# Kernel tuning notes

Measured on AMD Instinct MI355X. Metric: run time of the kernel, lower is better.

The kernel has to match this reference:

```python
import jax, jax.numpy as jnp
import numpy as np

H = 1024      # hidden_size
NH = 16       # num_attention_heads
KV = 4        # num_key_value_heads
HD = 64       # head_dim
E = 16        # num_experts
K = 2         # num_experts_per_tok
F = 1024      # moe_intermediate_size
EPS = 1e-6
THETA = 10000.0
B, S = 2, 1024


def rmsnorm(x, w):
    v = x.astype(jnp.float32)
    v = v * jax.lax.rsqrt(jnp.mean(v * v, axis=-1, keepdims=True) + EPS)
    return (v * w).astype(x.dtype)


def rotate_half(x):
    h = x.shape[-1] // 2
    return jnp.concatenate([-x[..., h:], x[..., :h]], axis=-1)


def setup_inputs() -> dict:
    key = jax.random.key(0)
    ks = jax.random.split(key, 12)
    s = 0.02
    return {
        "hidden_states": jax.random.normal(ks[0], (B, S, H), jnp.float32),
        "position_ids": jnp.broadcast_to(jnp.arange(S, dtype=jnp.int32), (B, S)),
        "ln1_w": jnp.ones((H,), jnp.float32),
        "ln2_w": jnp.ones((H,), jnp.float32),
        "q_w": jax.random.normal(ks[1], (NH * HD, H), jnp.float32) * s,
        "k_w": jax.random.normal(ks[2], (KV * HD, H), jnp.float32) * s,
        "v_w": jax.random.normal(ks[3], (KV * HD, H), jnp.float32) * s,
        "o_w": jax.random.normal(ks[4], (H, NH * HD), jnp.float32) * s,
        "qn_w": jnp.ones((HD,), jnp.float32),
        "kn_w": jnp.ones((HD,), jnp.float32),
        "gate_w": jax.random.normal(ks[5], (E, H), jnp.float32) * s,
        "w_gate": jax.random.normal(ks[6], (E, F, H), jnp.float32) * s,
        "w_up": jax.random.normal(ks[7], (E, F, H), jnp.float32) * s,
        "w_down": jax.random.normal(ks[8], (E, H, F), jnp.float32) * s,
    }


def reference(hidden_states, position_ids, ln1_w, ln2_w, q_w, k_w, v_w, o_w,
              qn_w, kn_w, gate_w, w_gate, w_up, w_down):
    b, s, _ = hidden_states.shape
    # ---- attention (pre-norm, bidirectional, GQA, RoPE, q/k RMSNorm) ----
    h = rmsnorm(hidden_states, ln1_w)
    q = (h @ q_w.T).reshape(b, s, NH, HD)
    k = (h @ k_w.T).reshape(b, s, KV, HD)
    v = (h @ v_w.T).reshape(b, s, KV, HD)
    q = jnp.swapaxes(rmsnorm(q, qn_w), 1, 2)   # [b,NH,s,HD]
    k = jnp.swapaxes(rmsnorm(k, kn_w), 1, 2)   # [b,KV,s,HD]
    v = jnp.swapaxes(v, 1, 2)
    inv_freq = 1.0 / (THETA ** (jnp.arange(0, HD, 2, dtype=jnp.float32) / HD))
    freqs = position_ids.astype(jnp.float32)[..., None] * inv_freq  # [b,s,HD/2]
    emb = jnp.concatenate([freqs, freqs], axis=-1)                  # [b,s,HD]
    cos = jnp.cos(emb)[:, None]                                     # [b,1,s,HD]
    sin = jnp.sin(emb)[:, None]
    q = q * cos + rotate_half(q) * sin
    k = k * cos + rotate_half(k) * sin
    rep = NH // KV
    k = jnp.repeat(k, rep, axis=1)
    v = jnp.repeat(v, rep, axis=1)
    scores = jnp.einsum('bhqd,bhkd->bhqk', q, k) * (HD ** -0.5)
    attn = jax.nn.softmax(scores.astype(jnp.float32), axis=-1).astype(q.dtype)
    o = jnp.einsum('bhqk,bhkd->bhqd', attn, v)
    o = jnp.swapaxes(o, 1, 2).reshape(b, s, NH * HD) @ o_w.T
    x1 = hidden_states + o
    # ---- sparse MoE (pre-norm, top-k routing, silu-gated experts) ----
    h2 = rmsnorm(x1, ln2_w)
    xf = h2.reshape(-1, H)                                  # [T,H]
    logits = xf @ gate_w.T                                  # [T,E]
    probs = jax.nn.softmax(logits.astype(jnp.float32), axis=-1)
    w, sel = jax.lax.top_k(probs, K)                        # [T,K]
    w = w / jnp.sum(w, axis=-1, keepdims=True)              # norm_topk_prob
    T = xf.shape[0]
    # combine weights scattered into dense [T,E] (zero for unselected experts)
    cw = jnp.zeros((T, E), jnp.float32).at[jnp.arange(T)[:, None], sel].add(w)
    g = jnp.einsum('th,efh->tef', xf, w_gate)
    u = jnp.einsum('th,efh->tef', xf, w_up)
    a = jax.nn.silu(g) * u
    y = jnp.einsum('tef,ehf,te->th', a, w_down, cw.astype(xf.dtype))
    out = x1 + y.reshape(b, s, H)
    return out, logits.reshape(b, s, E)
```

## Files before the change

### kernel.cpp

```cpp
#include <hip/hip_runtime.h>
#include <hip/hip_bf16.h>
#include <math.h>

typedef __bf16 bf16x8 __attribute__((ext_vector_type(8)));
typedef float f32x4 __attribute__((ext_vector_type(4)));

constexpr int HID = 1024;
constexpr int NHEAD = 16;
constexpr int NKV = 4;
constexpr int HDIM = 64;
constexpr int NEXP = 16;
constexpr int FFD = 1024;
constexpr int NB = 2;
constexpr int SEQ = 1024;
constexpr int TOK = NB * SEQ;
constexpr int QKV_N = NHEAD * HDIM + 2 * NKV * HDIM;
constexpr float RMS_EPS = 1e-6f;
constexpr int LDP = 40;
constexpr int PL = 64 * LDP;

__device__ __forceinline__ void split2(float x, __bf16& h1, __bf16& h2) {
  h1 = (__bf16)x;
  h2 = (__bf16)(x - (float)h1);
}

__device__ __forceinline__ void mfma_step3(const __bf16* sm, int wr, int wc,
                                           int lm, int lq, f32x4 (&acc)[2][2]) {
  int ao0 = (wr + lm) * LDP + lq * 8, ao1 = (wr + 16 + lm) * LDP + lq * 8;
  int bo0 = (wc + lm) * LDP + lq * 8, bo1 = (wc + 16 + lm) * LDP + lq * 8;
  bf16x8 a10 = *(const bf16x8*)(sm + ao0),          a11 = *(const bf16x8*)(sm + ao1);
  bf16x8 a20 = *(const bf16x8*)(sm + PL + ao0),     a21 = *(const bf16x8*)(sm + PL + ao1);
  bf16x8 b10 = *(const bf16x8*)(sm + 2 * PL + bo0), b11 = *(const bf16x8*)(sm + 2 * PL + bo1);
  bf16x8 b20 = *(const bf16x8*)(sm + 3 * PL + bo0), b21 = *(const bf16x8*)(sm + 3 * PL + bo1);
#define MF(A, B, i, j) acc[i][j] = __builtin_amdgcn_mfma_f32_16x16x32_bf16(A, B, acc[i][j], 0, 0, 0)
  MF(a10, b10, 0, 0); MF(a10, b11, 0, 1); MF(a11, b10, 1, 0); MF(a11, b11, 1, 1);
  MF(a10, b20, 0, 0); MF(a10, b21, 0, 1); MF(a11, b20, 1, 0); MF(a11, b21, 1, 1);
  MF(a20, b10, 0, 0); MF(a20, b11, 0, 1); MF(a21, b10, 1, 0); MF(a21, b11, 1, 1);
#undef MF
}

__device__ __forceinline__ void cvt8(__bf16* dst, float4 f0, float4 f1) {
  __bf16 tmp[8] __attribute__((aligned(16))) = {
      (__bf16)f0.x, (__bf16)f0.y, (__bf16)f0.z, (__bf16)f0.w,
      (__bf16)f1.x, (__bf16)f1.y, (__bf16)f1.z, (__bf16)f1.w};
  *(int4*)dst = *(const int4*)tmp;
}


__global__ __launch_bounds__(256) void split2_kernel(
    const float* __restrict__ src, __bf16* __restrict__ p1,
    __bf16* __restrict__ p2, int n) {
  int i = (blockIdx.x * 256 + threadIdx.x) * 4;
  if (i >= n) return;
  float4 v = *(const float4*)(src + i);
  __bf16 t1[4] __attribute__((aligned(8))), t2[4] __attribute__((aligned(8)));
  split2(v.x, t1[0], t2[0]);
  split2(v.y, t1[1], t2[1]);
  split2(v.z, t1[2], t2[2]);
  split2(v.w, t1[3], t2[3]);
  *(int2*)(p1 + i) = *(const int2*)t1;
  *(int2*)(p2 + i) = *(const int2*)t2;
}

__global__ __launch_bounds__(256) void rmsnorm_split2_kernel(
    const float* __restrict__ x, const float* __restrict__ w,
    __bf16* __restrict__ p1, __bf16* __restrict__ p2) {
  int row = blockIdx.x;
  const float* xr = x + (size_t)row * HID;
  float4 v = ((const float4*)xr)[threadIdx.x];
  float ss = v.x * v.x + v.y * v.y + v.z * v.z + v.w * v.w;
  for (int off = 32; off; off >>= 1) ss += __shfl_xor(ss, off);
  __shared__ float red[4];
  int lane = threadIdx.x & 63, wid = threadIdx.x >> 6;
  if (lane == 0) red[wid] = ss;
  __syncthreads();
  float tot = red[0] + red[1] + red[2] + red[3];
  float scale = rsqrtf(tot / (float)HID + RMS_EPS);
  float4 wv = ((const float4*)w)[threadIdx.x];
  float o[4] = {v.x * scale * wv.x, v.y * scale * wv.y,
                v.z * scale * wv.z, v.w * scale * wv.w};
  __bf16 t1[4] __attribute__((aligned(8))), t2[4] __attribute__((aligned(8)));
#pragma unroll
  for (int i = 0; i < 4; i++) split2(o[i], t1[i], t2[i]);
  size_t idx = (size_t)row * HID + threadIdx.x * 4;
  *(int2*)(p1 + idx) = *(const int2*)t1;
  *(int2*)(p2 + idx) = *(const int2*)t2;
}

__global__ __launch_bounds__(256) void rmsnorm_dual_kernel(
    const float* __restrict__ x, const float* __restrict__ w,
    float* __restrict__ outf, __bf16* __restrict__ outb) {
  int row = blockIdx.x;
  const float* xr = x + (size_t)row * HID;
  float4 v = ((const float4*)xr)[threadIdx.x];
  float ss = v.x * v.x + v.y * v.y + v.z * v.z + v.w * v.w;
  for (int off = 32; off; off >>= 1) ss += __shfl_xor(ss, off);
  __shared__ float red[4];
  int lane = threadIdx.x & 63, wid = threadIdx.x >> 6;
  if (lane == 0) red[wid] = ss;
  __syncthreads();
  float tot = red[0] + red[1] + red[2] + red[3];
  float scale = rsqrtf(tot / (float)HID + RMS_EPS);
  float4 wv = ((const float4*)w)[threadIdx.x];
  float o[4] = {v.x * scale * wv.x, v.y * scale * wv.y,
                v.z * scale * wv.z, v.w * scale * wv.w};
  size_t idx = (size_t)row * HID + threadIdx.x * 4;
  *(float4*)(outf + idx) = *(const float4*)o;
  __bf16 tb[4] __attribute__((aligned(8)));
#pragma unroll
  for (int i = 0; i < 4; i++) tb[i] = (__bf16)o[i];
  *(int2*)(outb + idx) = *(const int2*)tb;
}

__global__ __launch_bounds__(256) void rope_split_kernel(
    const float* __restrict__ qkv, const int* __restrict__ pos_ids,
    const float* __restrict__ qn_w, const float* __restrict__ kn_w,
    __bf16* __restrict__ qp1, __bf16* __restrict__ qp2,
    __bf16* __restrict__ kp1, __bf16* __restrict__ kp2,
    __bf16* __restrict__ vp1, __bf16* __restrict__ vp2) {
  int t = blockIdx.x;
  int b = t >> 10, s = t & 1023;
  int lane = threadIdx.x & 63, w = threadIdx.x >> 6;
  float pos = (float)pos_ids[t];
  int fi = lane & 31;
  float inv = powf(10000.0f, -((float)(2 * fi)) / 64.0f);
  float cs = cosf(pos * inv), sn = sinf(pos * inv);
  for (int i = 0; i < 6; i++) {
    int hh = w + 4 * i;
    float val = qkv[(size_t)t * QKV_N + hh * 64 + lane];
    __bf16 h1, h2;
    if (hh < 20) {
      float ss = val * val;
      for (int off = 32; off; off >>= 1) ss += __shfl_xor(ss, off);
      float scale = rsqrtf(ss / 64.0f + RMS_EPS);
      float wgt = (hh < 16) ? qn_w[lane] : kn_w[lane];
      val = val * scale * wgt;
      float partner = __shfl_xor(val, 32);
      float rot = (lane < 32) ? -partner : partner;
      val = val * cs + rot * sn;
      split2(val, h1, h2);
      if (hh < 16) {
        size_t idx = (((size_t)b * NHEAD + hh) * SEQ + s) * HDIM + lane;
        qp1[idx] = h1; qp2[idx] = h2;
      } else {
        size_t idx = (((size_t)b * NKV + (hh - 16)) * SEQ + s) * HDIM + lane;
        kp1[idx] = h1; kp2[idx] = h2;
      }
    } else {
      split2(val, h1, h2);
      size_t idx = (((size_t)b * NKV + (hh - 20)) * HDIM + lane) * SEQ + s;
      vp1[idx] = h1; vp2[idx] = h2;
    }
  }
}

__global__ __launch_bounds__(256) void softmax2_kernel(
    const float* __restrict__ sf,
    __bf16* __restrict__ p1, __bf16* __restrict__ p2) {
  size_t roff = (size_t)blockIdx.x * SEQ;
  int tid = threadIdx.x;
  float4 v4 = *(const float4*)(sf + roff + tid * 4);
  float v[4] = {v4.x, v4.y, v4.z, v4.w};
  float mx = fmaxf(fmaxf(v[0], v[1]), fmaxf(v[2], v[3]));
  for (int off = 32; off; off >>= 1) mx = fmaxf(mx, __shfl_xor(mx, off));
  __shared__ float red[4], red2[4];
  int lane = tid & 63, wid = tid >> 6;
  if (lane == 0) red[wid] = mx;
  __syncthreads();
  mx = fmaxf(fmaxf(red[0], red[1]), fmaxf(red[2], red[3]));
  float e[4], sum = 0.f;
#pragma unroll
  for (int i = 0; i < 4; i++) { e[i] = expf(v[i] - mx); sum += e[i]; }
  for (int off = 32; off; off >>= 1) sum += __shfl_xor(sum, off);
  if (lane == 0) red2[wid] = sum;
  __syncthreads();
  sum = red2[0] + red2[1] + red2[2] + red2[3];
  float invs = 1.0f / sum;
  __bf16 t1[4] __attribute__((aligned(8))), t2[4] __attribute__((aligned(8)));
#pragma unroll
  for (int i = 0; i < 4; i++) split2(e[i] * invs, t1[i], t2[i]);
  *(int2*)(p1 + roff + tid * 4) = *(const int2*)t1;
  *(int2*)(p2 + roff + tid * 4) = *(const int2*)t2;
}


__global__ __launch_bounds__(256) void gemm_qkv4(
    const __bf16* __restrict__ a1, const __bf16* __restrict__ a2,
    const __bf16* __restrict__ b1, const __bf16* __restrict__ b2,
    float* __restrict__ qkv) {
  int m0 = blockIdx.x * 64, n0 = blockIdx.y * 64;
  __shared__ __bf16 sm[4 * PL];
  int tid = threadIdx.x, r = tid >> 2, c8 = (tid & 3) * 8;
  size_t aoff = (size_t)(m0 + r) * HID + c8, boff = (size_t)(n0 + r) * HID + c8;
  f32x4 acc[2][2] = {};
  int lane = tid & 63, wid = tid >> 6;
  int wr = (wid >> 1) * 32, wc = (wid & 1) * 32, lq = lane >> 4, lm = lane & 15;
  int sidx = r * LDP + c8;
  int4 ra1, ra2, rb1, rb2;
  auto preload = [&](int k0) {
    ra1 = *(const int4*)(a1 + aoff + k0);
    ra2 = *(const int4*)(a2 + aoff + k0);
    rb1 = *(const int4*)(b1 + boff + k0);
    rb2 = *(const int4*)(b2 + boff + k0);
  };
  auto stage = [&]() {
    *(int4*)&sm[0 * PL + sidx] = ra1;
    *(int4*)&sm[1 * PL + sidx] = ra2;
    *(int4*)&sm[2 * PL + sidx] = rb1;
    *(int4*)&sm[3 * PL + sidx] = rb2;
  };
  preload(0); stage();
  for (int k0 = 0; k0 < HID; k0 += 32) {
    __syncthreads();
    if (k0 + 32 < HID) preload(k0 + 32);
    mfma_step3(sm, wr, wc, lm, lq, acc);
    __syncthreads();
    if (k0 + 32 < HID) stage();
  }
#pragma unroll
  for (int mt = 0; mt < 2; mt++)
#pragma unroll
    for (int nt = 0; nt < 2; nt++)
#pragma unroll
      for (int i = 0; i < 4; i++) {
        int gm = m0 + wr + mt * 16 + lq * 4 + i;
        int gc = n0 + wc + nt * 16 + lm;
        qkv[(size_t)gm * QKV_N + gc] = acc[mt][nt][i];
      }
}

__global__ __launch_bounds__(256) void gemm_scores4(
    const __bf16* __restrict__ qp1, const __bf16* __restrict__ qp2,
    const __bf16* __restrict__ kp1, const __bf16* __restrict__ kp2,
    float* __restrict__ sf, int b, int h0) {
  int hz = blockIdx.z, h = h0 + hz;
  int m0 = blockIdx.x * 64, n0 = blockIdx.y * 64;
  size_t qbase = ((size_t)(b * NHEAD + h)) * SEQ * HDIM;
  size_t kbase = ((size_t)(b * NKV + (h >> 2))) * SEQ * HDIM;
  __shared__ __bf16 sm[4 * PL];
  int tid = threadIdx.x, r = tid >> 2, c8 = (tid & 3) * 8;
  size_t aoff = qbase + (size_t)(m0 + r) * HDIM + c8;
  size_t boff = kbase + (size_t)(n0 + r) * HDIM + c8;
  f32x4 acc[2][2] = {};
  int lane = tid & 63, wid = tid >> 6;
  int wr = (wid >> 1) * 32, wc = (wid & 1) * 32, lq = lane >> 4, lm = lane & 15;
  int sidx = r * LDP + c8;
  int4 ra1, ra2, rb1, rb2;
  auto preload = [&](int k0) {
    ra1 = *(const int4*)(qp1 + aoff + k0);
    ra2 = *(const int4*)(qp2 + aoff + k0);
    rb1 = *(const int4*)(kp1 + boff + k0);
    rb2 = *(const int4*)(kp2 + boff + k0);
  };
  auto stage = [&]() {
    *(int4*)&sm[0 * PL + sidx] = ra1;
    *(int4*)&sm[1 * PL + sidx] = ra2;
    *(int4*)&sm[2 * PL + sidx] = rb1;
    *(int4*)&sm[3 * PL + sidx] = rb2;
  };
  preload(0); stage();
  for (int k0 = 0; k0 < HDIM; k0 += 32) {
    __syncthreads();
    if (k0 + 32 < HDIM) preload(k0 + 32);
    mfma_step3(sm, wr, wc, lm, lq, acc);
    __syncthreads();
    if (k0 + 32 < HDIM) stage();
  }
#pragma unroll
  for (int mt = 0; mt < 2; mt++)
#pragma unroll
    for (int nt = 0; nt < 2; nt++)
#pragma unroll
      for (int i = 0; i < 4; i++) {
        int gm = m0 + wr + mt * 16 + lq * 4 + i;
        int gc = n0 + wc + nt * 16 + lm;
        size_t idx = ((size_t)hz * SEQ + gm) * SEQ + gc;
        sf[idx] = acc[mt][nt][i] * 0.125f;
      }
}

__global__ __launch_bounds__(256) void gemm_pv4(
    const __bf16* __restrict__ s1, const __bf16* __restrict__ s2,
    const __bf16* __restrict__ vp1, const __bf16* __restrict__ vp2,
    __bf16* __restrict__ o1, __bf16* __restrict__ o2,
    int b, int h0) {
  int hz = blockIdx.z, h = h0 + hz;
  int m0 = blockIdx.x * 64;
  size_t pbase = (size_t)hz * SEQ * SEQ;
  size_t vbase = ((size_t)(b * NKV + (h >> 2))) * HDIM * SEQ;
  __shared__ __bf16 sm[4 * PL];
  int tid = threadIdx.x, r = tid >> 2, c8 = (tid & 3) * 8;
  size_t aoff = pbase + (size_t)(m0 + r) * SEQ + c8;
  size_t boff = vbase + (size_t)r * SEQ + c8;
  f32x4 acc[2][2] = {};
  int lane = tid & 63, wid = tid >> 6;
  int wr = (wid >> 1) * 32, wc = (wid & 1) * 32, lq = lane >> 4, lm = lane & 15;
  int sidx = r * LDP + c8;
  int4 ra1, ra2, rb1, rb2;
  auto preload = [&](int k0) {
    ra1 = *(const int4*)(s1 + aoff + k0);
    ra2 = *(const int4*)(s2 + aoff + k0);
    rb1 = *(const int4*)(vp1 + boff + k0);
    rb2 = *(const int4*)(vp2 + boff + k0);
  };
  auto stage = [&]() {
    *(int4*)&sm[0 * PL + sidx] = ra1;
    *(int4*)&sm[1 * PL + sidx] = ra2;
    *(int4*)&sm[2 * PL + sidx] = rb1;
    *(int4*)&sm[3 * PL + sidx] = rb2;
  };
  preload(0); stage();
  for (int k0 = 0; k0 < SEQ; k0 += 32) {
    __syncthreads();
    if (k0 + 32 < SEQ) preload(k0 + 32);
    mfma_step3(sm, wr, wc, lm, lq, acc);
    __syncthreads();
    if (k0 + 32 < SEQ) stage();
  }
#pragma unroll
  for (int mt = 0; mt < 2; mt++)
#pragma unroll
    for (int nt = 0; nt < 2; nt++)
#pragma unroll
      for (int i = 0; i < 4; i++) {
        int gm = m0 + wr + mt * 16 + lq * 4 + i;
        int gc = wc + nt * 16 + lm;
        size_t idx = ((size_t)(b * SEQ + gm)) * HID + h * 64 + gc;
        __bf16 h1_, h2_;
        split2(acc[mt][nt][i], h1_, h2_);
        o1[idx] = h1_; o2[idx] = h2_;
      }
}

__global__ __launch_bounds__(256) void gemm_oproj4(
    const __bf16* __restrict__ a1, const __bf16* __restrict__ a2,
    const __bf16* __restrict__ b1, const __bf16* __restrict__ b2,
    const float* __restrict__ hidden, float* __restrict__ x1, float* __restrict__ outp) {
  int m0 = blockIdx.x * 64, n0 = blockIdx.y * 64;
  __shared__ __bf16 sm[4 * PL];
  int tid = threadIdx.x, r = tid >> 2, c8 = (tid & 3) * 8;
  size_t aoff = (size_t)(m0 + r) * HID + c8, boff = (size_t)(n0 + r) * HID + c8;
  f32x4 acc[2][2] = {};
  int lane = tid & 63, wid = tid >> 6;
  int wr = (wid >> 1) * 32, wc = (wid & 1) * 32, lq = lane >> 4, lm = lane & 15;
  int sidx = r * LDP + c8;
  int4 ra1, ra2, rb1, rb2;
  auto preload = [&](int k0) {
    ra1 = *(const int4*)(a1 + aoff + k0);
    ra2 = *(const int4*)(a2 + aoff + k0);
    rb1 = *(const int4*)(b1 + boff + k0);
    rb2 = *(const int4*)(b2 + boff + k0);
  };
  auto stage = [&]() {
    *(int4*)&sm[0 * PL + sidx] = ra1;
    *(int4*)&sm[1 * PL + sidx] = ra2;
    *(int4*)&sm[2 * PL + sidx] = rb1;
    *(int4*)&sm[3 * PL + sidx] = rb2;
  };
  preload(0); stage();
  for (int k0 = 0; k0 < HID; k0 += 32) {
    __syncthreads();
    if (k0 + 32 < HID) preload(k0 + 32);
    mfma_step3(sm, wr, wc, lm, lq, acc);
    __syncthreads();
    if (k0 + 32 < HID) stage();
  }
#pragma unroll
  for (int mt = 0; mt < 2; mt++)
#pragma unroll
    for (int nt = 0; nt < 2; nt++)
#pragma unroll
      for (int i = 0; i < 4; i++) {
        int gm = m0 + wr + mt * 16 + lq * 4 + i;
        int gc = n0 + wc + nt * 16 + lm;
        size_t idx = (size_t)gm * HID + gc;
        float val = hidden[idx] + acc[mt][nt][i];
        x1[idx] = val;
        outp[idx] = val;
      }
}


__global__ void zero_cnt_kernel(int* cnt) {
  if (threadIdx.x < NEXP) cnt[threadIdx.x] = 0;
}

__global__ __launch_bounds__(64) void gating_kernel(
    const float* __restrict__ h2f, const float* __restrict__ gw,
    float* __restrict__ logits_out, int* __restrict__ cnt,
    int* __restrict__ list, float* __restrict__ wt) {
  int t = blockIdx.x;
  int lane = threadIdx.x;
  const float* xr = h2f + (size_t)t * HID;
  float part[NEXP] = {};
  for (int k = lane; k < HID; k += 64) {
    float xv = xr[k];
#pragma unroll
    for (int e = 0; e < NEXP; e++) part[e] += xv * gw[e * HID + k];
  }
#pragma unroll
  for (int e = 0; e < NEXP; e++)
    for (int off = 32; off; off >>= 1) part[e] += __shfl_xor(part[e], off);
  if (lane < NEXP) logits_out[(size_t)t * NEXP + lane] = part[lane];
  float mx = part[0];
#pragma unroll
  for (int e = 1; e < NEXP; e++) mx = fmaxf(mx, part[e]);
  float pe[NEXP];
#pragma unroll
  for (int e = 0; e < NEXP; e++) pe[e] = expf(part[e] - mx);
  int e0 = 0; float p0 = pe[0];
#pragma unroll
  for (int e = 1; e < NEXP; e++) if (pe[e] > p0) { p0 = pe[e]; e0 = e; }
  int e1 = -1; float p1 = -1.f;
#pragma unroll
  for (int e = 0; e < NEXP; e++) if (e != e0 && pe[e] > p1) { p1 = pe[e]; e1 = e; }
  float wsum = p0 + p1;
  if (lane == 0) {
    int pos0 = atomicAdd(&cnt[e0], 1);
    list[e0 * TOK + pos0] = t;
    wt[e0 * TOK + pos0] = p0 / wsum;
    int pos1 = atomicAdd(&cnt[e1], 1);
    list[e1 * TOK + pos1] = t;
    wt[e1 * TOK + pos1] = p1 / wsum;
  }
}

__global__ void scan_kernel(const int* __restrict__ cnt, int* __restrict__ base) {
  if (threadIdx.x == 0 && blockIdx.x == 0) {
    int acc = 0;
    for (int e = 0; e < NEXP; e++) { base[e] = acc; acc += cnt[e]; }
    base[NEXP] = acc;
  }
}

__global__ __launch_bounds__(256) void gemm_gateup3(
    const __bf16* __restrict__ h2, const float* __restrict__ w_gate,
    const float* __restrict__ w_up, const int* __restrict__ cnt,
    const int* __restrict__ base, const int* __restrict__ list,
    __bf16* __restrict__ aws) {
  int e = blockIdx.z;
  int ce = cnt[e];
  int m0 = blockIdx.y * 64;
  if (m0 >= ce) return;
  int n0 = blockIdx.x * 64;
  int be = base[e];
  __shared__ __bf16 As[2][PL], Bg[2][PL], Bu[2][PL];
  int tid = threadIdx.x, r = tid >> 2, c8 = (tid & 3) * 8;
  int ridx = m0 + r; if (ridx >= ce) ridx = ce - 1;
  const __bf16* arow = h2 + (size_t)list[e * TOK + ridx] * HID + c8;
  const float* bgrow = w_gate + ((size_t)e * FFD + n0 + r) * HID + c8;
  const float* burow = w_up + ((size_t)e * FFD + n0 + r) * HID + c8;
  int lane = tid & 63, wid = tid >> 6;
  int wr = (wid >> 1) * 32, wc = (wid & 1) * 32, lq = lane >> 4, lm = lane & 15;
  int sidx = r * LDP + c8;
  f32x4 ag[2][2] = {}, au[2][2] = {};
  int4 ra; float4 rg0, rg1, ru0, ru1;
  auto preload = [&](int k0) {
    ra = *(const int4*)(arow + k0);
    rg0 = *(const float4*)(bgrow + k0);
    rg1 = *(const float4*)(bgrow + k0 + 4);
    ru0 = *(const float4*)(burow + k0);
    ru1 = *(const float4*)(burow + k0 + 4);
  };
  auto stage = [&](int p) {
    *(int4*)&As[p][sidx] = ra;
    cvt8(&Bg[p][sidx], rg0, rg1);
    cvt8(&Bu[p][sidx], ru0, ru1);
  };
  preload(0);
  stage(0);
  preload(32);
  __syncthreads();
  int p = 0;
  for (int k0 = 0; k0 < HID; k0 += 32, p ^= 1) {
    bf16x8 a0 = *(const bf16x8*)(&As[p][(wr + lm) * LDP + lq * 8]);
    bf16x8 a1 = *(const bf16x8*)(&As[p][(wr + 16 + lm) * LDP + lq * 8]);
    bf16x8 g0 = *(const bf16x8*)(&Bg[p][(wc + lm) * LDP + lq * 8]);
    bf16x8 g1 = *(const bf16x8*)(&Bg[p][(wc + 16 + lm) * LDP + lq * 8]);
    bf16x8 u0 = *(const bf16x8*)(&Bu[p][(wc + lm) * LDP + lq * 8]);
    bf16x8 u1 = *(const bf16x8*)(&Bu[p][(wc + 16 + lm) * LDP + lq * 8]);
    if (k0 + 32 < HID) {
      stage(p ^ 1);
      preload(k0 + 64 < HID ? k0 + 64 : 0);
    }
    ag[0][0] = __builtin_amdgcn_mfma_f32_16x16x32_bf16(a0, g0, ag[0][0], 0, 0, 0);
    ag[0][1] = __builtin_amdgcn_mfma_f32_16x16x32_bf16(a0, g1, ag[0][1], 0, 0, 0);
    ag[1][0] = __builtin_amdgcn_mfma_f32_16x16x32_bf16(a1, g0, ag[1][0], 0, 0, 0);
    ag[1][1] = __builtin_amdgcn_mfma_f32_16x16x32_bf16(a1, g1, ag[1][1], 0, 0, 0);
    au[0][0] = __builtin_amdgcn_mfma_f32_16x16x32_bf16(a0, u0, au[0][0], 0, 0, 0);
    au[0][1] = __builtin_amdgcn_mfma_f32_16x16x32_bf16(a0, u1, au[0][1], 0, 0, 0);
    au[1][0] = __builtin_amdgcn_mfma_f32_16x16x32_bf16(a1, u0, au[1][0], 0, 0, 0);
    au[1][1] = __builtin_amdgcn_mfma_f32_16x16x32_bf16(a1, u1, au[1][1], 0, 0, 0);
    __syncthreads();
  }
#pragma unroll
  for (int mt = 0; mt < 2; mt++)
#pragma unroll
    for (int nt = 0; nt < 2; nt++)
#pragma unroll
      for (int i = 0; i < 4; i++) {
        int lrow = m0 + wr + mt * 16 + lq * 4 + i;
        if (lrow < ce) {
          int gc = n0 + wc + nt * 16 + lm;
          float g = ag[mt][nt][i], u = au[mt][nt][i];
          float a = g / (1.0f + expf(-g)) * u;
          aws[((size_t)(be + lrow)) * FFD + gc] = (__bf16)a;
        }
      }
}

__global__ __launch_bounds__(256) void gemm_down3(
    const __bf16* __restrict__ aws, const float* __restrict__ w_down,
    const int* __restrict__ cnt, const int* __restrict__ base,
    const int* __restrict__ list, const float* __restrict__ wt,
    float* __restrict__ outp) {
  int e = blockIdx.z;
  int ce = cnt[e];
  int m0 = blockIdx.y * 64;
  if (m0 >= ce) return;
  int n0 = blockIdx.x * 64;
  int be = base[e];
  __shared__ __bf16 As[2][PL], Bs[2][PL];
  int tid = threadIdx.x, r = tid >> 2, c8 = (tid & 3) * 8;
  int ridx = m0 + r; if (ridx >= ce) ridx = ce - 1;
  const __bf16* arow = aws + (size_t)(be + ridx) * FFD + c8;
  const float* brow = w_down + ((size_t)e * HID + n0 + r) * FFD + c8;
  int lane = tid & 63, wid = tid >> 6;
  int wr = (wid >> 1) * 32, wc = (wid & 1) * 32, lq = lane >> 4, lm = lane & 15;
  int sidx = r * LDP + c8;
  f32x4 acc[2][2] = {};
  int4 ra; float4 rb0, rb1;
  auto preload = [&](int k0) {
    ra = *(const int4*)(arow + k0);
    rb0 = *(const float4*)(brow + k0);
    rb1 = *(const float4*)(brow + k0 + 4);
  };
  auto stage = [&](int p) {
    *(int4*)&As[p][sidx] = ra;
    cvt8(&Bs[p][sidx], rb0, rb1);
  };
  preload(0);
  stage(0);
  preload(32);
  __syncthreads();
  int p = 0;
  for (int k0 = 0; k0 < FFD; k0 += 32, p ^= 1) {
    bf16x8 a0 = *(const bf16x8*)(&As[p][(wr + lm) * LDP + lq * 8]);
    bf16x8 a1 = *(const bf16x8*)(&As[p][(wr + 16 + lm) * LDP + lq * 8]);
    bf16x8 b0 = *(const bf16x8*)(&Bs[p][(wc + lm) * LDP + lq * 8]);
    bf16x8 b1 = *(const bf16x8*)(&Bs[p][(wc + 16 + lm) * LDP + lq * 8]);
    if (k0 + 32 < FFD) {
      stage(p ^ 1);
      preload(k0 + 64 < FFD ? k0 + 64 : 0);
    }
    acc[0][0] = __builtin_amdgcn_mfma_f32_16x16x32_bf16(a0, b0, acc[0][0], 0, 0, 0);
    acc[0][1] = __builtin_amdgcn_mfma_f32_16x16x32_bf16(a0, b1, acc[0][1], 0, 0, 0);
    acc[1][0] = __builtin_amdgcn_mfma_f32_16x16x32_bf16(a1, b0, acc[1][0], 0, 0, 0);
    acc[1][1] = __builtin_amdgcn_mfma_f32_16x16x32_bf16(a1, b1, acc[1][1], 0, 0, 0);
    __syncthreads();
  }
#pragma unroll
  for (int mt = 0; mt < 2; mt++)
#pragma unroll
    for (int nt = 0; nt < 2; nt++)
#pragma unroll
      for (int i = 0; i < 4; i++) {
        int lrow = m0 + wr + mt * 16 + lq * 4 + i;
        if (lrow < ce) {
          int gc = n0 + wc + nt * 16 + lm;
          int tok = list[e * TOK + lrow];
          float wgt = wt[e * TOK + lrow];
          atomicAdd(&outp[(size_t)tok * HID + gc], wgt * acc[mt][nt][i]);
        }
      }
}


extern "C" void kernel_launch(void* const* d_in, const int* in_sizes, int n_in,
                              void* d_out, int out_size, void* d_ws, size_t ws_size,
                              hipStream_t stream) {
  const float* hidden = (const float*)d_in[0];
  const int* pos_ids = (const int*)d_in[1];
  const float* ln1_w = (const float*)d_in[2];
  const float* ln2_w = (const float*)d_in[3];
  const float* q_w = (const float*)d_in[4];
  const float* k_w = (const float*)d_in[5];
  const float* v_w = (const float*)d_in[6];
  const float* o_w = (const float*)d_in[7];
  const float* qn_w = (const float*)d_in[8];
  const float* kn_w = (const float*)d_in[9];
  const float* gate_w = (const float*)d_in[10];
  const float* w_gate = (const float*)d_in[11];
  const float* w_up = (const float*)d_in[12];
  const float* w_down = (const float*)d_in[13];
  float* outp = (float*)d_out;
  float* logits_out = outp + (size_t)TOK * HID;

  char* ws = (char*)d_ws;
  size_t off = 0;
  auto alloc = [&](size_t bytes) {
    void* p = ws + off;
    off += (bytes + 255) & ~(size_t)255;
    return p;
  };
  const size_t NWQ = (size_t)QKV_N * HID, NOW = (size_t)HID * HID;
  __bf16* wqp1 = (__bf16*)alloc(NWQ * 2); __bf16* wqp2 = (__bf16*)alloc(NWQ * 2);
  __bf16* owp1 = (__bf16*)alloc(NOW * 2); __bf16* owp2 = (__bf16*)alloc(NOW * 2);
  const size_t NH1 = (size_t)TOK * HID;
  __bf16* h1p1 = (__bf16*)alloc(NH1 * 2); __bf16* h1p2 = (__bf16*)alloc(NH1 * 2);
  float* qkvf = (float*)alloc((size_t)TOK * QKV_N * 4);
  const size_t NQ = (size_t)NB * NHEAD * SEQ * HDIM, NK = (size_t)NB * NKV * SEQ * HDIM;
  __bf16* qp1 = (__bf16*)alloc(NQ * 2); __bf16* qp2 = (__bf16*)alloc(NQ * 2);
  __bf16* kp1 = (__bf16*)alloc(NK * 2); __bf16* kp2 = (__bf16*)alloc(NK * 2);
  __bf16* vp1 = (__bf16*)alloc(NK * 2); __bf16* vp2 = (__bf16*)alloc(NK * 2);
  size_t fixed_rest = NH1 * 2 * 2  + NH1 * 4 * 2  + NH1 * 2  +
                      NEXP * 4 * 2 + (size_t)NEXP * TOK * 8 +
                      (size_t)TOK * 2 * FFD * 2 + (1 << 20);
  size_t avail = (ws_size > off + fixed_rest) ? (ws_size - off - fixed_rest) : 0;
  int hch = (avail >= (size_t)16 * SEQ * SEQ * 8) ? 16 : 8;
  const size_t NP = (size_t)hch * SEQ * SEQ;
  float* spf = (float*)alloc(NP * 4);
  __bf16* sp1 = (__bf16*)alloc(NP * 2); __bf16* sp2 = (__bf16*)alloc(NP * 2);
  __bf16* op1 = (__bf16*)alloc(NH1 * 2); __bf16* op2 = (__bf16*)alloc(NH1 * 2);
  float* x1 = (float*)alloc(NH1 * 4);
  float* h2f = (float*)alloc(NH1 * 4);
  __bf16* h2b = (__bf16*)alloc(NH1 * 2);
  int* cnt = (int*)alloc(NEXP * 4);
  int* base = (int*)alloc((NEXP + 1) * 4);
  int* list = (int*)alloc((size_t)NEXP * TOK * 4);
  float* wt = (float*)alloc((size_t)NEXP * TOK * 4);
  __bf16* aws = (__bf16*)alloc((size_t)TOK * 2 * FFD * 2);
  (void)in_sizes; (void)n_in; (void)out_size;

  split2_kernel<<<1024, 256, 0, stream>>>(q_w, wqp1, wqp2, 1024 * 1024);
  split2_kernel<<<256, 256, 0, stream>>>(k_w, wqp1 + 1024 * 1024, wqp2 + 1024 * 1024,
                                         256 * 1024);
  split2_kernel<<<256, 256, 0, stream>>>(v_w, wqp1 + 1280 * 1024, wqp2 + 1280 * 1024,
                                         256 * 1024);
  split2_kernel<<<1024, 256, 0, stream>>>(o_w, owp1, owp2, 1024 * 1024);

  rmsnorm_split2_kernel<<<TOK, 256, 0, stream>>>(hidden, ln1_w, h1p1, h1p2);
  gemm_qkv4<<<dim3(TOK / 64, QKV_N / 64), 256, 0, stream>>>(
      h1p1, h1p2, wqp1, wqp2, qkvf);
  rope_split_kernel<<<TOK, 256, 0, stream>>>(qkvf, pos_ids, qn_w, kn_w,
                                             qp1, qp2, kp1, kp2, vp1, vp2);
  for (int b = 0; b < NB; b++)
    for (int hc = 0; hc < NHEAD / hch; hc++) {
      int h0 = hc * hch;
      gemm_scores4<<<dim3(SEQ / 64, SEQ / 64, hch), 256, 0, stream>>>(
          qp1, qp2, kp1, kp2, spf, b, h0);
      softmax2_kernel<<<hch * SEQ, 256, 0, stream>>>(spf, sp1, sp2);
      gemm_pv4<<<dim3(SEQ / 64, 1, hch), 256, 0, stream>>>(
          sp1, sp2, vp1, vp2, op1, op2, b, h0);
    }
  gemm_oproj4<<<dim3(TOK / 64, HID / 64), 256, 0, stream>>>(
      op1, op2, owp1, owp2, hidden, x1, outp);

  rmsnorm_dual_kernel<<<TOK, 256, 0, stream>>>(x1, ln2_w, h2f, h2b);
  zero_cnt_kernel<<<1, 64, 0, stream>>>(cnt);
  gating_kernel<<<TOK, 64, 0, stream>>>(h2f, gate_w, logits_out, cnt, list, wt);
  scan_kernel<<<1, 1, 0, stream>>>(cnt, base);
  gemm_gateup3<<<dim3(FFD / 64, TOK / 64, NEXP), 256, 0, stream>>>(
      h2b, w_gate, w_up, cnt, base, list, aws);
  gemm_down3<<<dim3(HID / 64, TOK / 64, NEXP), 256, 0, stream>>>(
      aws, w_down, cnt, base, list, wt, outp);
}
```

Baseline: 564.5 us.

## Deepen GEMM pipelines with double-buffered LDS and two-deep register prefetch

The QKV, PV and O-projection GEMMs move from a single LDS buffer with two barriers per K-step to double-buffered shared memory with one barrier per step. All five GEMM kernels, including the MoE gate/up and down kernels, now keep two register prefetch sets alive, so global loads are issued two tiles ahead. The aim is to hide global memory latency and cut barrier stalls. In exchange it raises register and LDS pressure, which may reduce occupancy.

```diff
diff --git a/kernel.cpp b/kernel.cpp
--- a/kernel.cpp
+++ b/kernel.cpp
@@ -189,33 +189,43 @@
     const __bf16* __restrict__ b1, const __bf16* __restrict__ b2,
     float* __restrict__ qkv) {
   int m0 = blockIdx.x * 64, n0 = blockIdx.y * 64;
-  __shared__ __bf16 sm[4 * PL];
+  __shared__ __bf16 sm[2][4 * PL];
   int tid = threadIdx.x, r = tid >> 2, c8 = (tid & 3) * 8;
   size_t aoff = (size_t)(m0 + r) * HID + c8, boff = (size_t)(n0 + r) * HID + c8;
   f32x4 acc[2][2] = {};
   int lane = tid & 63, wid = tid >> 6;
   int wr = (wid >> 1) * 32, wc = (wid & 1) * 32, lq = lane >> 4, lm = lane & 15;
   int sidx = r * LDP + c8;
-  int4 ra1, ra2, rb1, rb2;
-  auto preload = [&](int k0) {
-    ra1 = *(const int4*)(a1 + aoff + k0);
-    ra2 = *(const int4*)(a2 + aoff + k0);
-    rb1 = *(const int4*)(b1 + boff + k0);
-    rb2 = *(const int4*)(b2 + boff + k0);
-  };
-  auto stage = [&]() {
-    *(int4*)&sm[0 * PL + sidx] = ra1;
-    *(int4*)&sm[1 * PL + sidx] = ra2;
-    *(int4*)&sm[2 * PL + sidx] = rb1;
-    *(int4*)&sm[3 * PL + sidx] = rb2;
-  };
-  preload(0); stage();
-  for (int k0 = 0; k0 < HID; k0 += 32) {
-    __syncthreads();
-    if (k0 + 32 < HID) preload(k0 + 32);
-    mfma_step3(sm, wr, wc, lm, lq, acc);
-    __syncthreads();
-    if (k0 + 32 < HID) stage();
+  int4 rA1, rA2, rA3, rA4, rB1, rB2, rB3, rB4;
+  auto preloadA = [&](int k0) {
+    rA1 = *(const int4*)(a1 + aoff + k0); rA2 = *(const int4*)(a2 + aoff + k0);
+    rA3 = *(const int4*)(b1 + boff + k0); rA4 = *(const int4*)(b2 + boff + k0);
+  };
+  auto preloadB = [&](int k0) {
+    rB1 = *(const int4*)(a1 + aoff + k0); rB2 = *(const int4*)(a2 + aoff + k0);
+    rB3 = *(const int4*)(b1 + boff + k0); rB4 = *(const int4*)(b2 + boff + k0);
+  };
+  auto stageA = [&](int p) {
+    *(int4*)&sm[p][0 * PL + sidx] = rA1; *(int4*)&sm[p][1 * PL + sidx] = rA2;
+    *(int4*)&sm[p][2 * PL + sidx] = rA3; *(int4*)&sm[p][3 * PL + sidx] = rA4;
+  };
+  auto stageB = [&](int p) {
+    *(int4*)&sm[p][0 * PL + sidx] = rB1; *(int4*)&sm[p][1 * PL + sidx] = rB2;
+    *(int4*)&sm[p][2 * PL + sidx] = rB3; *(int4*)&sm[p][3 * PL + sidx] = rB4;
+  };
+  preloadA(0); stageA(0);
+  preloadA(32); preloadB(64);
+  __syncthreads();
+  int p = 0;
+  for (int k0 = 0; k0 < HID; k0 += 64) {
+    if (k0 + 32 < HID) stageA(p ^ 1);
+    if (k0 + 96 < HID) preloadA(k0 + 96);
+    mfma_step3(sm[p], wr, wc, lm, lq, acc);
+    __syncthreads(); p ^= 1;
+    if (k0 + 64 < HID) stageB(p ^ 1);
+    if (k0 + 128 < HID) preloadB(k0 + 128);
+    mfma_step3(sm[p], wr, wc, lm, lq, acc);
+    __syncthreads(); p ^= 1;
   }
 #pragma unroll
   for (int mt = 0; mt < 2; mt++)
@@ -288,7 +298,7 @@
   int m0 = blockIdx.x * 64;
   size_t pbase = (size_t)hz * SEQ * SEQ;
   size_t vbase = ((size_t)(b * NKV + (h >> 2))) * HDIM * SEQ;
-  __shared__ __bf16 sm[4 * PL];
+  __shared__ __bf16 sm[2][4 * PL];
   int tid = threadIdx.x, r = tid >> 2, c8 = (tid & 3) * 8;
   size_t aoff = pbase + (size_t)(m0 + r) * SEQ + c8;
   size_t boff = vbase + (size_t)r * SEQ + c8;
@@ -296,26 +306,36 @@
   int lane = tid & 63, wid = tid >> 6;
   int wr = (wid >> 1) * 32, wc = (wid & 1) * 32, lq = lane >> 4, lm = lane & 15;
   int sidx = r * LDP + c8;
-  int4 ra1, ra2, rb1, rb2;
-  auto preload = [&](int k0) {
-    ra1 = *(const int4*)(s1 + aoff + k0);
-    ra2 = *(const int4*)(s2 + aoff + k0);
-    rb1 = *(const int4*)(vp1 + boff + k0);
-    rb2 = *(const int4*)(vp2 + boff + k0);
-  };
-  auto stage = [&]() {
-    *(int4*)&sm[0 * PL + sidx] = ra1;
-    *(int4*)&sm[1 * PL + sidx] = ra2;
-    *(int4*)&sm[2 * PL + sidx] = rb1;
-    *(int4*)&sm[3 * PL + sidx] = rb2;
-  };
-  preload(0); stage();
-  for (int k0 = 0; k0 < SEQ; k0 += 32) {
-    __syncthreads();
-    if (k0 + 32 < SEQ) preload(k0 + 32);
-    mfma_step3(sm, wr, wc, lm, lq, acc);
-    __syncthreads();
-    if (k0 + 32 < SEQ) stage();
+  int4 rA1, rA2, rA3, rA4, rB1, rB2, rB3, rB4;
+  auto preloadA = [&](int k0) {
+    rA1 = *(const int4*)(s1 + aoff + k0);  rA2 = *(const int4*)(s2 + aoff + k0);
+    rA3 = *(const int4*)(vp1 + boff + k0); rA4 = *(const int4*)(vp2 + boff + k0);
+  };
+  auto preloadB = [&](int k0) {
+    rB1 = *(const int4*)(s1 + aoff + k0);  rB2 = *(const int4*)(s2 + aoff + k0);
+    rB3 = *(const int4*)(vp1 + boff + k0); rB4 = *(const int4*)(vp2 + boff + k0);
+  };
+  auto stageA = [&](int p) {
+    *(int4*)&sm[p][0 * PL + sidx] = rA1; *(int4*)&sm[p][1 * PL + sidx] = rA2;
+    *(int4*)&sm[p][2 * PL + sidx] = rA3; *(int4*)&sm[p][3 * PL + sidx] = rA4;
+  };
+  auto stageB = [&](int p) {
+    *(int4*)&sm[p][0 * PL + sidx] = rB1; *(int4*)&sm[p][1 * PL + sidx] = rB2;
+    *(int4*)&sm[p][2 * PL + sidx] = rB3; *(int4*)&sm[p][3 * PL + sidx] = rB4;
+  };
+  preloadA(0); stageA(0);
+  preloadA(32); preloadB(64);
+  __syncthreads();
+  int p = 0;
+  for (int k0 = 0; k0 < SEQ; k0 += 64) {
+    if (k0 + 32 < SEQ) stageA(p ^ 1);
+    if (k0 + 96 < SEQ) preloadA(k0 + 96);
+    mfma_step3(sm[p], wr, wc, lm, lq, acc);
+    __syncthreads(); p ^= 1;
+    if (k0 + 64 < SEQ) stageB(p ^ 1);
+    if (k0 + 128 < SEQ) preloadB(k0 + 128);
+    mfma_step3(sm[p], wr, wc, lm, lq, acc);
+    __syncthreads(); p ^= 1;
   }
 #pragma unroll
   for (int mt = 0; mt < 2; mt++)
@@ -337,33 +357,43 @@
     const __bf16* __restrict__ b1, const __bf16* __restrict__ b2,
     const float* __restrict__ hidden, float* __restrict__ x1, float* __restrict__ outp) {
   int m0 = blockIdx.x * 64, n0 = blockIdx.y * 64;
-  __shared__ __bf16 sm[4 * PL];
+  __shared__ __bf16 sm[2][4 * PL];
   int tid = threadIdx.x, r = tid >> 2, c8 = (tid & 3) * 8;
   size_t aoff = (size_t)(m0 + r) * HID + c8, boff = (size_t)(n0 + r) * HID + c8;
   f32x4 acc[2][2] = {};
   int lane = tid & 63, wid = tid >> 6;
   int wr = (wid >> 1) * 32, wc = (wid & 1) * 32, lq = lane >> 4, lm = lane & 15;
   int sidx = r * LDP + c8;
-  int4 ra1, ra2, rb1, rb2;
-  auto preload = [&](int k0) {
-    ra1 = *(const int4*)(a1 + aoff + k0);
-    ra2 = *(const int4*)(a2 + aoff + k0);
-    rb1 = *(const int4*)(b1 + boff + k0);
-    rb2 = *(const int4*)(b2 + boff + k0);
-  };
-  auto stage = [&]() {
-    *(int4*)&sm[0 * PL + sidx] = ra1;
-    *(int4*)&sm[1 * PL + sidx] = ra2;
-    *(int4*)&sm[2 * PL + sidx] = rb1;
-    *(int4*)&sm[3 * PL + sidx] = rb2;
-  };
-  preload(0); stage();
-  for (int k0 = 0; k0 < HID; k0 += 32) {
-    __syncthreads();
-    if (k0 + 32 < HID) preload(k0 + 32);
-    mfma_step3(sm, wr, wc, lm, lq, acc);
-    __syncthreads();
-    if (k0 + 32 < HID) stage();
+  int4 rA1, rA2, rA3, rA4, rB1, rB2, rB3, rB4;
+  auto preloadA = [&](int k0) {
+    rA1 = *(const int4*)(a1 + aoff + k0); rA2 = *(const int4*)(a2 + aoff + k0);
+    rA3 = *(const int4*)(b1 + boff + k0); rA4 = *(const int4*)(b2 + boff + k0);
+  };
+  auto preloadB = [&](int k0) {
+    rB1 = *(const int4*)(a1 + aoff + k0); rB2 = *(const int4*)(a2 + aoff + k0);
+    rB3 = *(const int4*)(b1 + boff + k0); rB4 = *(const int4*)(b2 + boff + k0);
+  };
+  auto stageA = [&](int p) {
+    *(int4*)&sm[p][0 * PL + sidx] = rA1; *(int4*)&sm[p][1 * PL + sidx] = rA2;
+    *(int4*)&sm[p][2 * PL + sidx] = rA3; *(int4*)&sm[p][3 * PL + sidx] = rA4;
+  };
+  auto stageB = [&](int p) {
+    *(int4*)&sm[p][0 * PL + sidx] = rB1; *(int4*)&sm[p][1 * PL + sidx] = rB2;
+    *(int4*)&sm[p][2 * PL + sidx] = rB3; *(int4*)&sm[p][3 * PL + sidx] = rB4;
+  };
+  preloadA(0); stageA(0);
+  preloadA(32); preloadB(64);
+  __syncthreads();
+  int p = 0;
+  for (int k0 = 0; k0 < HID; k0 += 64) {
+    if (k0 + 32 < HID) stageA(p ^ 1);
+    if (k0 + 96 < HID) preloadA(k0 + 96);
+    mfma_step3(sm[p], wr, wc, lm, lq, acc);
+    __syncthreads(); p ^= 1;
+    if (k0 + 64 < HID) stageB(p ^ 1);
+    if (k0 + 128 < HID) preloadB(k0 + 128);
+    mfma_step3(sm[p], wr, wc, lm, lq, acc);
+    __syncthreads(); p ^= 1;
   }
 #pragma unroll
   for (int mt = 0; mt < 2; mt++)
@@ -454,35 +484,34 @@
   int wr = (wid >> 1) * 32, wc = (wid & 1) * 32, lq = lane >> 4, lm = lane & 15;
   int sidx = r * LDP + c8;
   f32x4 ag[2][2] = {}, au[2][2] = {};
-  int4 ra; float4 rg0, rg1, ru0, ru1;
-  auto preload = [&](int k0) {
-    ra = *(const int4*)(arow + k0);
-    rg0 = *(const float4*)(bgrow + k0);
-    rg1 = *(const float4*)(bgrow + k0 + 4);
-    ru0 = *(const float4*)(burow + k0);
-    ru1 = *(const float4*)(burow + k0 + 4);
-  };
-  auto stage = [&](int p) {
-    *(int4*)&As[p][sidx] = ra;
-    cvt8(&Bg[p][sidx], rg0, rg1);
-    cvt8(&Bu[p][sidx], ru0, ru1);
-  };
-  preload(0);
-  stage(0);
-  preload(32);
-  __syncthreads();
-  int p = 0;
-  for (int k0 = 0; k0 < HID; k0 += 32, p ^= 1) {
+  int4 raA, raB; float4 rgA0, rgA1, ruA0, ruA1, rgB0, rgB1, ruB0, ruB1;
+  auto preloadA = [&](int k0) {
+    raA = *(const int4*)(arow + k0);
+    rgA0 = *(const float4*)(bgrow + k0); rgA1 = *(const float4*)(bgrow + k0 + 4);
+    ruA0 = *(const float4*)(burow + k0); ruA1 = *(const float4*)(burow + k0 + 4);
+  };
+  auto preloadB = [&](int k0) {
+    raB = *(const int4*)(arow + k0);
+    rgB0 = *(const float4*)(bgrow + k0); rgB1 = *(const float4*)(bgrow + k0 + 4);
+    ruB0 = *(const float4*)(burow + k0); ruB1 = *(const float4*)(burow + k0 + 4);
+  };
+  auto stageA = [&](int p) {
+    *(int4*)&As[p][sidx] = raA;
+    cvt8(&Bg[p][sidx], rgA0, rgA1);
+    cvt8(&Bu[p][sidx], ruA0, ruA1);
+  };
+  auto stageB = [&](int p) {
+    *(int4*)&As[p][sidx] = raB;
+    cvt8(&Bg[p][sidx], rgB0, rgB1);
+    cvt8(&Bu[p][sidx], ruB0, ruB1);
+  };
+  auto compute = [&](int p) {
     bf16x8 a0 = *(const bf16x8*)(&As[p][(wr + lm) * LDP + lq * 8]);
     bf16x8 a1 = *(const bf16x8*)(&As[p][(wr + 16 + lm) * LDP + lq * 8]);
     bf16x8 g0 = *(const bf16x8*)(&Bg[p][(wc + lm) * LDP + lq * 8]);
     bf16x8 g1 = *(const bf16x8*)(&Bg[p][(wc + 16 + lm) * LDP + lq * 8]);
     bf16x8 u0 = *(const bf16x8*)(&Bu[p][(wc + lm) * LDP + lq * 8]);
     bf16x8 u1 = *(const bf16x8*)(&Bu[p][(wc + 16 + lm) * LDP + lq * 8]);
-    if (k0 + 32 < HID) {
-      stage(p ^ 1);
-      preload(k0 + 64 < HID ? k0 + 64 : 0);
-    }
     ag[0][0] = __builtin_amdgcn_mfma_f32_16x16x32_bf16(a0, g0, ag[0][0], 0, 0, 0);
     ag[0][1] = __builtin_amdgcn_mfma_f32_16x16x32_bf16(a0, g1, ag[0][1], 0, 0, 0);
     ag[1][0] = __builtin_amdgcn_mfma_f32_16x16x32_bf16(a1, g0, ag[1][0], 0, 0, 0);
@@ -491,7 +520,20 @@
     au[0][1] = __builtin_amdgcn_mfma_f32_16x16x32_bf16(a0, u1, au[0][1], 0, 0, 0);
     au[1][0] = __builtin_amdgcn_mfma_f32_16x16x32_bf16(a1, u0, au[1][0], 0, 0, 0);
     au[1][1] = __builtin_amdgcn_mfma_f32_16x16x32_bf16(a1, u1, au[1][1], 0, 0, 0);
-    __syncthreads();
+  };
+  preloadA(0); stageA(0);
+  preloadA(32); preloadB(64);
+  __syncthreads();
+  int p = 0;
+  for (int k0 = 0; k0 < HID; k0 += 64) {
+    if (k0 + 32 < HID) stageA(p ^ 1);
+    if (k0 + 96 < HID) preloadA(k0 + 96);
+    compute(p);
+    __syncthreads(); p ^= 1;
+    if (k0 + 64 < HID) stageB(p ^ 1);
+    if (k0 + 128 < HID) preloadB(k0 + 128);
+    compute(p);
+    __syncthreads(); p ^= 1;
   }
 #pragma unroll
   for (int mt = 0; mt < 2; mt++)
@@ -529,35 +571,46 @@
   int wr = (wid >> 1) * 32, wc = (wid & 1) * 32, lq = lane >> 4, lm = lane & 15;
   int sidx = r * LDP + c8;
   f32x4 acc[2][2] = {};
-  int4 ra; float4 rb0, rb1;
-  auto preload = [&](int k0) {
-    ra = *(const int4*)(arow + k0);
-    rb0 = *(const float4*)(brow + k0);
-    rb1 = *(const float4*)(brow + k0 + 4);
-  };
-  auto stage = [&](int p) {
-    *(int4*)&As[p][sidx] = ra;
-    cvt8(&Bs[p][sidx], rb0, rb1);
-  };
-  preload(0);
-  stage(0);
-  preload(32);
-  __syncthreads();
-  int p = 0;
-  for (int k0 = 0; k0 < FFD; k0 += 32, p ^= 1) {
+  int4 raA, raB; float4 rbA0, rbA1, rbB0, rbB1;
+  auto preloadA = [&](int k0) {
+    raA = *(const int4*)(arow + k0);
+    rbA0 = *(const float4*)(brow + k0); rbA1 = *(const float4*)(brow + k0 + 4);
+  };
+  auto preloadB = [&](int k0) {
+    raB = *(const int4*)(arow + k0);
+    rbB0 = *(const float4*)(brow + k0); rbB1 = *(const float4*)(brow + k0 + 4);
+  };
+  auto stageA = [&](int p) {
+    *(int4*)&As[p][sidx] = raA;
+    cvt8(&Bs[p][sidx], rbA0, rbA1);
+  };
+  auto stageB = [&](int p) {
+    *(int4*)&As[p][sidx] = raB;
+    cvt8(&Bs[p][sidx], rbB0, rbB1);
+  };
+  auto compute = [&](int p) {
     bf16x8 a0 = *(const bf16x8*)(&As[p][(wr + lm) * LDP + lq * 8]);
     bf16x8 a1 = *(const bf16x8*)(&As[p][(wr + 16 + lm) * LDP + lq * 8]);
     bf16x8 b0 = *(const bf16x8*)(&Bs[p][(wc + lm) * LDP + lq * 8]);
     bf16x8 b1 = *(const bf16x8*)(&Bs[p][(wc + 16 + lm) * LDP + lq * 8]);
-    if (k0 + 32 < FFD) {
-      stage(p ^ 1);
-      preload(k0 + 64 < FFD ? k0 + 64 : 0);
-    }
     acc[0][0] = __builtin_amdgcn_mfma_f32_16x16x32_bf16(a0, b0, acc[0][0], 0, 0, 0);
     acc[0][1] = __builtin_amdgcn_mfma_f32_16x16x32_bf16(a0, b1, acc[0][1], 0, 0, 0);
     acc[1][0] = __builtin_amdgcn_mfma_f32_16x16x32_bf16(a1, b0, acc[1][0], 0, 0, 0);
     acc[1][1] = __builtin_amdgcn_mfma_f32_16x16x32_bf16(a1, b1, acc[1][1], 0, 0, 0);
-    __syncthreads();
+  };
+  preloadA(0); stageA(0);
+  preloadA(32); preloadB(64);
+  __syncthreads();
+  int p = 0;
+  for (int k0 = 0; k0 < FFD; k0 += 64) {
+    if (k0 + 32 < FFD) stageA(p ^ 1);
+    if (k0 + 96 < FFD) preloadA(k0 + 96);
+    compute(p);
+    __syncthreads(); p ^= 1;
+    if (k0 + 64 < FFD) stageB(p ^ 1);
+    if (k0 + 128 < FFD) preloadB(k0 + 128);
+    compute(p);
+    __syncthreads(); p ^= 1;
   }
 #pragma unroll
   for (int mt = 0; mt < 2; mt++)
```

Result: faster. 542.3 us (-3.9%).
